# Optimization experiments

Hardware: AMD Instinct MI355X
Metric: run time of the kernel (lower is better)

The kernel has to match this reference:

```python
import jax, jax.numpy as jnp
import numpy as np

VOCAB = 32000
EMB = 10
HID = 256
CLS = 10
B = 1024
T = 256


def setup_inputs() -> dict:
    key = jax.random.key(0)
    ks = jax.random.split(key, 12)
    def w(k, shape):
        fan_in = shape[1]  # torch kaiming_normal_ (fan_in = size(1), gain=1 for 'linear')
        return jax.random.normal(k, shape, dtype=jnp.float32) / jnp.sqrt(jnp.float32(fan_in))
    inp = {
        "x": jax.random.randint(ks[0], (B, 1, T), 0, VOCAB, dtype=jnp.int32),
        "emb": jax.random.normal(ks[1], (VOCAB, EMB), dtype=jnp.float32),
        "Wgx": w(ks[2], (EMB, HID)), "Wgh": w(ks[3], (HID, HID)), "bg": jnp.zeros((HID,), jnp.float32),
        "Wix": w(ks[4], (EMB, HID)), "Wih": w(ks[5], (HID, HID)), "bi": jnp.zeros((HID,), jnp.float32),
        "Wfx": w(ks[6], (EMB, HID)), "Wfh": w(ks[7], (HID, HID)), "bf": jnp.zeros((HID,), jnp.float32),
        "Wox": w(ks[8], (EMB, HID)), "Woh": w(ks[9], (HID, HID)), "bo": jnp.zeros((HID,), jnp.float32),
        "Wph": w(ks[10], (HID, CLS)), "bp": jnp.zeros((CLS,), jnp.float32),
    }
    return inp


def reference(x, emb, Wgx, Wgh, bg, Wix, Wih, bi, Wfx, Wfh, bf, Wox, Woh, bo, Wph, bp):
    # Fuse the 4 gate projections into single matmuls (same math, concatenated).
    Wx = jnp.concatenate([Wgx, Wix, Wfx, Wox], axis=1)  # [EMB, 4H]
    Wh = jnp.concatenate([Wgh, Wih, Wfh, Woh], axis=1)  # [HID, 4H]
    b = jnp.concatenate([bg, bi, bf, bo], axis=0)       # [4H]
    H = Wgh.shape[0]
    tokens = x[:, 0, :].T  # [T, B] int

    def step(carry, tok_t):
        h, c = carry
        x_t = emb[tok_t]                       # [B, EMB]
        z = x_t @ Wx + h @ Wh + b              # [B, 4H]
        g = jnp.tanh(z[:, 0 * H:1 * H])
        i = jax.nn.sigmoid(z[:, 1 * H:2 * H])
        f = jax.nn.sigmoid(z[:, 2 * H:3 * H])
        o = jax.nn.sigmoid(z[:, 3 * H:4 * H])
        c = g * i + c * f
        h = jnp.tanh(c) * o
        return (h, c), None

    Bn = x.shape[0]
    h0 = jnp.zeros((Bn, H), dtype=emb.dtype)
    c0 = jnp.zeros((Bn, H), dtype=emb.dtype)
    (h, c), _ = jax.lax.scan(step, (h0, c0), tokens)
    return h @ Wph + bp  # [B, num_classes]
```

## Files before the change

### kernel.cpp

```cpp
#include <hip/hip_runtime.h>
#include <stdint.h>

#define T_STEPS 256
#define EMBD 10
#define NKIT 9
#define NBLK_K1 (64 * NKIT)
#define NBLK 256

typedef __attribute__((ext_vector_type(8))) short bf16x8;
typedef __attribute__((ext_vector_type(4))) float f32x4;
typedef __attribute__((ext_vector_type(4))) int   i32x4;

__device__ __forceinline__ unsigned short f2bf(float f) {
    union { float f; unsigned int u; } v; v.f = f;
    unsigned int u = v.u;
    unsigned int r = (u + 0x7FFFu + ((u >> 16) & 1u)) >> 16;
    return (unsigned short)r;
}
__device__ __forceinline__ float sig_fast(float x) {
    return __builtin_amdgcn_rcpf(1.0f + __builtin_amdgcn_exp2f(-1.4426950408889634f * x));
}
__device__ __forceinline__ float tanh_fast(float x) {
    return 1.0f - 2.0f * __builtin_amdgcn_rcpf(__builtin_amdgcn_exp2f(2.8853900817779268f * x) + 1.0f);
}
__device__ __forceinline__ f32x4 mfma_v(i32x4 a, i32x4 b, f32x4 c) {
    return __builtin_amdgcn_mfma_f32_16x16x32_bf16(
        __builtin_bit_cast(bf16x8, a), __builtin_bit_cast(bf16x8, b), c, 0, 0, 0);
}

__global__ __launch_bounds__(64) void build_wswz(
    const float* __restrict__ Wgx, const float* __restrict__ Wgh, const float* __restrict__ bg,
    const float* __restrict__ Wix, const float* __restrict__ Wih, const float* __restrict__ bi,
    const float* __restrict__ Wfx, const float* __restrict__ Wfh, const float* __restrict__ bf_,
    const float* __restrict__ Wox, const float* __restrict__ Woh, const float* __restrict__ bo,
    unsigned short* __restrict__ wswz, unsigned int* __restrict__ hxcz)
{
    {
        int4 z4 = {0, 0, 0, 0};
        size_t gid = (size_t)blockIdx.x * 64 + threadIdx.x;
        for (size_t i = gid; i < 131072; i += (size_t)NBLK_K1 * 64)
            ((int4*)hxcz)[i] = z4;
    }

    int g   = blockIdx.x / NKIT;
    int kit = blockIdx.x % NKIT;
    int lane = threadIdx.x;
    int n = g * 16 + (lane & 15);
    int q = n >> 8;
    int col = n & 255;
    const float* Wh = (q == 0) ? Wgh : (q == 1) ? Wih : (q == 2) ? Wfh : Woh;
    const float* Wx = (q == 0) ? Wgx : (q == 1) ? Wix : (q == 2) ? Wfx : Wox;
    const float* bb = (q == 0) ? bg  : (q == 1) ? bi  : (q == 2) ? bf_ : bo;
    int k0 = kit * 32 + (lane >> 4) * 8;

    int4 out;
    unsigned short* p = (unsigned short*)&out;
#pragma unroll
    for (int jx = 0; jx < 8; jx++) {
        int k = k0 + jx;
        float v = 0.0f;
        if (k < 256)             v = Wh[k * 256 + col];
        else if (k < 256 + EMBD) v = Wx[(k - 256) * 256 + col];
        else if (k == 266)       v = bb[col];
        p[jx] = f2bf(v);
    }
    ((int4*)wswz)[(kit * 64 + g) * 64 + lane] = out;
}

#define KIDX(s) ((s) == 7 ? 5 : (s))
#define BSRC(s, g) ((s) == 5 ? B_lds[(0 * 16 + (g) * 4 + j) * 64 + lane] \
                  : (s) == 6 ? B_lds[(1 * 16 + (g) * 4 + j) * 64 + lane] \
                  : breg[KIDX(s)][(g)])
#define DO_KIT(s) do { i32x4 a_ = ((const i32x4*)Ah_lds)[ah_rd + (s) * 4]; \
        acc0 = mfma_v(a_, BSRC(s, 0), acc0); \
        acc1 = mfma_v(a_, BSRC(s, 1), acc1); \
        acc2 = mfma_v(a_, BSRC(s, 2), acc2); \
        acc3 = mfma_v(a_, BSRC(s, 3), acc3); } while (0)

__global__ __launch_bounds__(256)
__attribute__((amdgpu_waves_per_eu(1)))
void lstm_main(
    const int*   __restrict__ xtok,
    const float* __restrict__ emb,
    const float* __restrict__ Wph,
    const float* __restrict__ bp,
    const unsigned short* __restrict__ wswz,
    unsigned long long* __restrict__ hxc,
    float* __restrict__ out)
{
    __shared__ __align__(16) unsigned short A8_lds[2][64 * 8];
    __shared__ __align__(16) i32x4 B_lds[2 * 16 * 64];
    __shared__ __align__(16) unsigned int Ah_lds[16 * 132];
    __shared__ float hbuf[16][68];
    __shared__ float outacc[160];

    const int tid  = threadIdx.x;
    const int j    = tid >> 6;
    const int lane = tid & 63;
    const int qq   = lane >> 4;
    const int col15 = lane & 15;
    const int blk  = blockIdx.x;
    const int gb   = blk & 63;
    const int hg   = blk >> 6;

    const int m_x = tid >> 4;
    const int e_x = tid & 15;

    const i32x4* Bg = (const i32x4*)wswz;

    i32x4 breg[7][4];
    {
        const int ks[7] = {0, 1, 2, 3, 4, 7, 8};
#pragma unroll
        for (int i = 0; i < 7; i++)
#pragma unroll
            for (int g = 0; g < 4; g++)
                breg[i][g] = Bg[(ks[i] * 64 + g * 16 + hg * 4 + j) * 64 + lane];
    }
    for (int i = tid; i < 2 * 16 * 64; i += 256) {
        int k   = i >> 10;
        int ntl = (i >> 6) & 15;
        int ln  = i & 63;
        int g_ = ntl >> 2, jj = ntl & 3;
        B_lds[i] = Bg[((5 + k) * 64 + g_ * 16 + hg * 4 + jj) * 64 + ln];
    }

    {
        int4 z4 = {0, 0, 0, 0};
        if (tid < 128) ((int4*)A8_lds)[tid] = z4;
    }
    __syncthreads();
    if (tid < 16) {
        A8_lds[0][(16 + tid) * 8 + 2] = 0x3F80;
        A8_lds[1][(16 + tid) * 8 + 2] = 0x3F80;
    }
    if (e_x < EMBD) {
        int tok = xtok[(gb * 16 + m_x) * T_STEPS + 0];
        float v = emb[tok * EMBD + e_x];
        A8_lds[0][(m_x + 16 * (e_x >> 3)) * 8 + (e_x & 7)] = f2bf(v);
    }
    __syncthreads();

    float c0 = 0.f, c1 = 0.f, c2 = 0.f, c3 = 0.f;

    const int ah_rd = (lane & 15) * 33 + (lane >> 4);
    const int c_loc = tid >> 2;
    const int rp0   = (tid & 3) * 2;
    const int rq0 = (hg + 1) & 3, rq1 = (hg + 2) & 3, rq2 = (hg + 3) & 3;
    const int c_own = hg * 64 + j * 16 + col15;
    unsigned short* AhS = (unsigned short*)Ah_lds;

    for (int t = 0; t < T_STEPS; t++) {
        const int p = t & 1, q = (t + 1) & 1;

        float xval = 0.0f;
        const bool do_x = (t < T_STEPS - 1) && (e_x < EMBD);
        if (t < T_STEPS - 1) {
            int tok = xtok[(gb * 16 + m_x) * T_STEPS + (t + 1)];
            if (e_x < EMBD) xval = emb[tok * EMBD + e_x];
        }

        const unsigned long long* hb = hxc + (size_t)(p * 64 + gb) * 2048;
        const unsigned long long* a0 = hb + (rq0 * 64 + c_loc) * 8 + rp0;
        const unsigned long long* a1 = hb + (rq1 * 64 + c_loc) * 8 + rp0;
        const unsigned long long* a2 = hb + (rq2 * 64 + c_loc) * 8 + rp0;
        i32x4 va, vb, vc;

        if (t > 0) {
            asm volatile("global_load_dwordx4 %0, %3, off sc1\n\t"
                         "global_load_dwordx4 %1, %4, off sc1\n\t"
                         "global_load_dwordx4 %2, %5, off sc1"
                         : "=&v"(va), "=&v"(vb), "=&v"(vc)
                         : "v"(a0), "v"(a1), "v"(a2) : "memory");
        }

        asm volatile("s_waitcnt lgkmcnt(0)" ::: "memory");
        __builtin_amdgcn_s_barrier();

        f32x4 acc0 = (f32x4){0.f, 0.f, 0.f, 0.f};
        f32x4 acc1 = (f32x4){0.f, 0.f, 0.f, 0.f};
        f32x4 acc2 = (f32x4){0.f, 0.f, 0.f, 0.f};
        f32x4 acc3 = (f32x4){0.f, 0.f, 0.f, 0.f};
        {
            i32x4 a8 = ((const i32x4*)A8_lds[p])[lane];
            acc0 = mfma_v(a8, breg[6][0], acc0);
            acc1 = mfma_v(a8, breg[6][1], acc1);
            acc2 = mfma_v(a8, breg[6][2], acc2);
            acc3 = mfma_v(a8, breg[6][3], acc3);
        }

        if (t > 0) {
            if      (hg == 0) { DO_KIT(0); DO_KIT(1); }
            else if (hg == 1) { DO_KIT(2); DO_KIT(3); }
            else if (hg == 2) { DO_KIT(4); DO_KIT(5); }
            else              { DO_KIT(6); DO_KIT(7); }

            asm volatile("s_waitcnt vmcnt(0)"
                         : "+v"(va), "+v"(vb), "+v"(vc) :: "memory");
            int spins = 0;
            while ((va.y != t || va.w != t || vb.y != t || vb.w != t ||
                    vc.y != t || vc.w != t) && spins < 20000) {
                ++spins;
                __builtin_amdgcn_s_sleep(1);
                asm volatile("global_load_dwordx4 %0, %3, off sc1\n\t"
                             "global_load_dwordx4 %1, %4, off sc1\n\t"
                             "global_load_dwordx4 %2, %5, off sc1\n\t"
                             "s_waitcnt vmcnt(0)"
                             : "=&v"(va), "=&v"(vb), "=&v"(vc)
                             : "v"(a0), "v"(a1), "v"(a2) : "memory");
            }
            {
                const int r0 = 2 * rp0;
                int cg0 = rq0 * 64 + c_loc;
                AhS[(r0 + 0) * 264 + cg0] = (unsigned short)(va.x & 0xffff);
                AhS[(r0 + 1) * 264 + cg0] = (unsigned short)((unsigned)va.x >> 16);
                AhS[(r0 + 2) * 264 + cg0] = (unsigned short)(va.z & 0xffff);
                AhS[(r0 + 3) * 264 + cg0] = (unsigned short)((unsigned)va.z >> 16);
                int cg1 = rq1 * 64 + c_loc;
                AhS[(r0 + 0) * 264 + cg1] = (unsigned short)(vb.x & 0xffff);
                AhS[(r0 + 1) * 264 + cg1] = (unsigned short)((unsigned)vb.x >> 16);
                AhS[(r0 + 2) * 264 + cg1] = (unsigned short)(vb.z & 0xffff);
                AhS[(r0 + 3) * 264 + cg1] = (unsigned short)((unsigned)vb.z >> 16);
                int cg2 = rq2 * 64 + c_loc;
                AhS[(r0 + 0) * 264 + cg2] = (unsigned short)(vc.x & 0xffff);
                AhS[(r0 + 1) * 264 + cg2] = (unsigned short)((unsigned)vc.x >> 16);
                AhS[(r0 + 2) * 264 + cg2] = (unsigned short)(vc.z & 0xffff);
                AhS[(r0 + 3) * 264 + cg2] = (unsigned short)((unsigned)vc.z >> 16);
            }
            asm volatile("s_waitcnt lgkmcnt(0)" ::: "memory");
            __builtin_amdgcn_s_barrier();

            if (hg != 0) { DO_KIT(0); DO_KIT(1); }
            if (hg != 1) { DO_KIT(2); DO_KIT(3); }
            if (hg != 2) { DO_KIT(4); DO_KIT(5); }
            if (hg != 3) { DO_KIT(6); DO_KIT(7); }
        }

        float h0, h1, h2, h3;
        {
            float gg, ii, ff, oo, cn;
            gg = tanh_fast(acc0[0]); ii = sig_fast(acc1[0]);
            ff = sig_fast(acc2[0]);  oo = sig_fast(acc3[0]);
            cn = gg * ii + c0 * ff; c0 = cn; h0 = tanh_fast(cn) * oo;
            gg = tanh_fast(acc0[1]); ii = sig_fast(acc1[1]);
            ff = sig_fast(acc2[1]);  oo = sig_fast(acc3[1]);
            cn = gg * ii + c1 * ff; c1 = cn; h1 = tanh_fast(cn) * oo;
            gg = tanh_fast(acc0[2]); ii = sig_fast(acc1[2]);
            ff = sig_fast(acc2[2]);  oo = sig_fast(acc3[2]);
            cn = gg * ii + c2 * ff; c2 = cn; h2 = tanh_fast(cn) * oo;
            gg = tanh_fast(acc0[3]); ii = sig_fast(acc1[3]);
            ff = sig_fast(acc2[3]);  oo = sig_fast(acc3[3]);
            cn = gg * ii + c3 * ff; c3 = cn; h3 = tanh_fast(cn) * oo;
        }

        if (t < T_STEPS - 1) {
            unsigned int p01, p23;
            asm("v_cvt_pk_bf16_f32 %0, %1, %2" : "=v"(p01) : "v"(h0), "v"(h1));
            asm("v_cvt_pk_bf16_f32 %0, %1, %2" : "=v"(p23) : "v"(h2), "v"(h3));
            AhS[(4 * qq + 0) * 264 + c_own] = (unsigned short)(p01 & 0xffff);
            AhS[(4 * qq + 1) * 264 + c_own] = (unsigned short)(p01 >> 16);
            AhS[(4 * qq + 2) * 264 + c_own] = (unsigned short)(p23 & 0xffff);
            AhS[(4 * qq + 3) * 264 + c_own] = (unsigned short)(p23 >> 16);
            if (do_x)
                A8_lds[q][(m_x + 16 * (e_x >> 3)) * 8 + (e_x & 7)] = f2bf(xval);
            i32x4 pv;
            pv.x = (int)p01; pv.y = t + 1; pv.z = (int)p23; pv.w = t + 1;
            unsigned long long* dst =
                hxc + (size_t)(q * 64 + gb) * 2048 + (size_t)c_own * 8 + 2 * qq;
            asm volatile("global_store_dwordx4 %0, %1, off sc1"
                         :: "v"(dst), "v"(pv) : "memory");
        } else {
            hbuf[4 * qq + 0][j * 16 + col15] = h0;
            hbuf[4 * qq + 1][j * 16 + col15] = h1;
            hbuf[4 * qq + 2][j * 16 + col15] = h2;
            hbuf[4 * qq + 3][j * 16 + col15] = h3;
            if (tid < 160) outacc[tid] = 0.0f;
            __syncthreads();
            if (tid < 160) {
                int m = tid / 10, cl = tid - m * 10;
                float s = 0.0f;
#pragma unroll 8
                for (int c = 0; c < 64; c++)
                    s += hbuf[m][c] * Wph[(hg * 64 + c) * 10 + cl];
                if (hg == 0) s += bp[cl];
                atomicAdd(&out[(gb * 16 + m) * 10 + cl], s);
            }
        }
    }
}

extern "C" void kernel_launch(void* const* d_in, const int* in_sizes, int n_in,
                              void* d_out, int out_size, void* d_ws, size_t ws_size,
                              hipStream_t stream) {
    const int*   x    = (const int*)  d_in[0];
    const float* emb  = (const float*)d_in[1];
    const float* Wgx  = (const float*)d_in[2];
    const float* Wgh  = (const float*)d_in[3];
    const float* bg   = (const float*)d_in[4];
    const float* Wix  = (const float*)d_in[5];
    const float* Wih  = (const float*)d_in[6];
    const float* bi   = (const float*)d_in[7];
    const float* Wfx  = (const float*)d_in[8];
    const float* Wfh  = (const float*)d_in[9];
    const float* bf_  = (const float*)d_in[10];
    const float* Wox  = (const float*)d_in[11];
    const float* Woh  = (const float*)d_in[12];
    const float* bo   = (const float*)d_in[13];
    const float* Wph  = (const float*)d_in[14];
    const float* bp   = (const float*)d_in[15];

    char* ws = (char*)d_ws;
    unsigned short*     wswz = (unsigned short*)ws;
    unsigned long long* hxc  = (unsigned long long*)(ws + 589824 + 4096);

    build_wswz<<<NBLK_K1, 64, 0, stream>>>(Wgx, Wgh, bg, Wix, Wih, bi,
                                           Wfx, Wfh, bf_, Wox, Woh, bo,
                                           wswz, (unsigned int*)hxc);
    lstm_main<<<NBLK, 256, 0, stream>>>(x, emb, Wph, bp, wswz, hxc,
                                        (float*)d_out);
}
```

Before: 555.2 us.

## Add dedicated poller wave to prefetch next-step hidden state into double-buffered LDS

Adds a fifth wave per block (320 threads) that spins on the global exchange buffer for the next step's hidden-state slices from the other three blocks and writes them into a double-buffered LDS tile. The four compute waves then run all eight MFMA k-iterations from LDS, with a single barrier per step. The aim is to take global polling and LDS scatter off the compute waves' critical path and drop the intra-step split and second barrier. In exchange there is an extra wave per block, doubled Ah LDS, and the waves_per_eu(1) attribute is removed, which may change register allocation for the 28 preloaded B fragments.

```diff
diff --git a/kernel.cpp b/kernel.cpp
--- a/kernel.cpp
+++ b/kernel.cpp
@@ -71,14 +71,13 @@
 #define BSRC(s, g) ((s) == 5 ? B_lds[(0 * 16 + (g) * 4 + j) * 64 + lane] \
                   : (s) == 6 ? B_lds[(1 * 16 + (g) * 4 + j) * 64 + lane] \
                   : breg[KIDX(s)][(g)])
-#define DO_KIT(s) do { i32x4 a_ = ((const i32x4*)Ah_lds)[ah_rd + (s) * 4]; \
+#define DO_KIT(s) do { i32x4 a_ = Ahp[ah_rd + (s) * 4]; \
         acc0 = mfma_v(a_, BSRC(s, 0), acc0); \
         acc1 = mfma_v(a_, BSRC(s, 1), acc1); \
         acc2 = mfma_v(a_, BSRC(s, 2), acc2); \
         acc3 = mfma_v(a_, BSRC(s, 3), acc3); } while (0)
 
-__global__ __launch_bounds__(256)
-__attribute__((amdgpu_waves_per_eu(1)))
+__global__ __launch_bounds__(320)
 void lstm_main(
     const int*   __restrict__ xtok,
     const float* __restrict__ emb,
@@ -90,9 +89,8 @@
 {
     __shared__ __align__(16) unsigned short A8_lds[2][64 * 8];
     __shared__ __align__(16) i32x4 B_lds[2 * 16 * 64];
-    __shared__ __align__(16) unsigned int Ah_lds[16 * 132];
+    __shared__ __align__(16) unsigned int Ah_lds[2][16 * 132];
     __shared__ float hbuf[16][68];
-    __shared__ float outacc[160];
 
     const int tid  = threadIdx.x;
     const int j    = tid >> 6;
@@ -102,6 +100,7 @@
     const int blk  = blockIdx.x;
     const int gb   = blk & 63;
     const int hg   = blk >> 6;
+    const bool is_comp = (tid < 256);
 
     const int m_x = tid >> 4;
     const int e_x = tid & 15;
@@ -109,7 +108,7 @@
     const i32x4* Bg = (const i32x4*)wswz;
 
     i32x4 breg[7][4];
-    {
+    if (is_comp) {
         const int ks[7] = {0, 1, 2, 3, 4, 7, 8};
 #pragma unroll
         for (int i = 0; i < 7; i++)
@@ -117,7 +116,7 @@
             for (int g = 0; g < 4; g++)
                 breg[i][g] = Bg[(ks[i] * 64 + g * 16 + hg * 4 + j) * 64 + lane];
     }
-    for (int i = tid; i < 2 * 16 * 64; i += 256) {
+    for (int i = tid; i < 2 * 16 * 64; i += 320) {
         int k   = i >> 10;
         int ntl = (i >> 6) & 15;
         int ln  = i & 63;
@@ -134,7 +133,7 @@
         A8_lds[0][(16 + tid) * 8 + 2] = 0x3F80;
         A8_lds[1][(16 + tid) * 8 + 2] = 0x3F80;
     }
-    if (e_x < EMBD) {
+    if (is_comp && e_x < EMBD) {
         int tok = xtok[(gb * 16 + m_x) * T_STEPS + 0];
         float v = emb[tok * EMBD + e_x];
         A8_lds[0][(m_x + 16 * (e_x >> 3)) * 8 + (e_x & 7)] = f2bf(v);
@@ -144,148 +143,138 @@
     float c0 = 0.f, c1 = 0.f, c2 = 0.f, c3 = 0.f;
 
     const int ah_rd = (lane & 15) * 33 + (lane >> 4);
-    const int c_loc = tid >> 2;
-    const int rp0   = (tid & 3) * 2;
-    const int rq0 = (hg + 1) & 3, rq1 = (hg + 2) & 3, rq2 = (hg + 3) & 3;
     const int c_own = hg * 64 + j * 16 + col15;
-    unsigned short* AhS = (unsigned short*)Ah_lds;
+
+    const int ptid = tid - 256;
+    int offv[12];
+#pragma unroll
+    for (int i = 0; i < 12; i++) {
+        int e   = ptid * 24 + 2 * i;
+        int rqi = e >> 9;
+        offv[i] = (rqi + (rqi >= hg ? 1 : 0)) * 512 + (e & 511);
+    }
 
     for (int t = 0; t < T_STEPS; t++) {
         const int p = t & 1, q = (t + 1) & 1;
 
-        float xval = 0.0f;
-        const bool do_x = (t < T_STEPS - 1) && (e_x < EMBD);
+        if (is_comp) {
+            float xval = 0.0f;
+            const bool do_x = (t < T_STEPS - 1) && (e_x < EMBD);
+            if (t < T_STEPS - 1) {
+                int tok = xtok[(gb * 16 + m_x) * T_STEPS + (t + 1)];
+                if (e_x < EMBD) xval = emb[tok * EMBD + e_x];
+            }
+
+            f32x4 acc0 = (f32x4){0.f, 0.f, 0.f, 0.f};
+            f32x4 acc1 = (f32x4){0.f, 0.f, 0.f, 0.f};
+            f32x4 acc2 = (f32x4){0.f, 0.f, 0.f, 0.f};
+            f32x4 acc3 = (f32x4){0.f, 0.f, 0.f, 0.f};
+            {
+                i32x4 a8 = ((const i32x4*)A8_lds[p])[lane];
+                acc0 = mfma_v(a8, breg[6][0], acc0);
+                acc1 = mfma_v(a8, breg[6][1], acc1);
+                acc2 = mfma_v(a8, breg[6][2], acc2);
+                acc3 = mfma_v(a8, breg[6][3], acc3);
+            }
+            if (t > 0) {
+                const i32x4* Ahp = (const i32x4*)Ah_lds[p];
+                DO_KIT(0); DO_KIT(1); DO_KIT(2); DO_KIT(3);
+                DO_KIT(4); DO_KIT(5); DO_KIT(6); DO_KIT(7);
+            }
+
+            float h0, h1, h2, h3;
+            {
+                float gg, ii, ff, oo, cn;
+                gg = tanh_fast(acc0[0]); ii = sig_fast(acc1[0]);
+                ff = sig_fast(acc2[0]);  oo = sig_fast(acc3[0]);
+                cn = gg * ii + c0 * ff; c0 = cn; h0 = tanh_fast(cn) * oo;
+                gg = tanh_fast(acc0[1]); ii = sig_fast(acc1[1]);
+                ff = sig_fast(acc2[1]);  oo = sig_fast(acc3[1]);
+                cn = gg * ii + c1 * ff; c1 = cn; h1 = tanh_fast(cn) * oo;
+                gg = tanh_fast(acc0[2]); ii = sig_fast(acc1[2]);
+                ff = sig_fast(acc2[2]);  oo = sig_fast(acc3[2]);
+                cn = gg * ii + c2 * ff; c2 = cn; h2 = tanh_fast(cn) * oo;
+                gg = tanh_fast(acc0[3]); ii = sig_fast(acc1[3]);
+                ff = sig_fast(acc2[3]);  oo = sig_fast(acc3[3]);
+                cn = gg * ii + c3 * ff; c3 = cn; h3 = tanh_fast(cn) * oo;
+            }
+
+            if (t < T_STEPS - 1) {
+                unsigned int p01, p23;
+                asm("v_cvt_pk_bf16_f32 %0, %1, %2" : "=v"(p01) : "v"(h0), "v"(h1));
+                asm("v_cvt_pk_bf16_f32 %0, %1, %2" : "=v"(p23) : "v"(h2), "v"(h3));
+                unsigned short* AqS = (unsigned short*)Ah_lds[q];
+                AqS[(4 * qq + 0) * 264 + c_own] = (unsigned short)(p01 & 0xffff);
+                AqS[(4 * qq + 1) * 264 + c_own] = (unsigned short)(p01 >> 16);
+                AqS[(4 * qq + 2) * 264 + c_own] = (unsigned short)(p23 & 0xffff);
+                AqS[(4 * qq + 3) * 264 + c_own] = (unsigned short)(p23 >> 16);
+                if (do_x)
+                    A8_lds[q][(m_x + 16 * (e_x >> 3)) * 8 + (e_x & 7)] = f2bf(xval);
+                i32x4 pv;
+                pv.x = (int)p01; pv.y = t + 1; pv.z = (int)p23; pv.w = t + 1;
+                unsigned long long* dst =
+                    hxc + (size_t)(q * 64 + gb) * 2048 + (size_t)c_own * 8 + 2 * qq;
+                asm volatile("global_store_dwordx4 %0, %1, off sc1"
+                             :: "v"(dst), "v"(pv) : "memory");
+            } else {
+                hbuf[4 * qq + 0][j * 16 + col15] = h0;
+                hbuf[4 * qq + 1][j * 16 + col15] = h1;
+                hbuf[4 * qq + 2][j * 16 + col15] = h2;
+                hbuf[4 * qq + 3][j * 16 + col15] = h3;
+            }
+        } else {
+            if (t < T_STEPS - 1) {
+                const unsigned long long* hbq =
+                    hxc + (size_t)(q * 64 + gb) * 2048;
+                const unsigned s_exp = (unsigned)(t + 1);
+                i32x4 pv[12];
+                int spins = 0;
+                for (;;) {
+#pragma unroll
+                    for (int i = 0; i < 12; i++)
+                        asm volatile("global_load_dwordx4 %0, %1, off sc1"
+                                     : "=&v"(pv[i]) : "v"(hbq + offv[i]) : "memory");
+                    asm volatile("s_waitcnt vmcnt(0)"
+                                 : "+v"(pv[0]), "+v"(pv[1]), "+v"(pv[2]), "+v"(pv[3]),
+                                   "+v"(pv[4]), "+v"(pv[5]), "+v"(pv[6]), "+v"(pv[7]),
+                                   "+v"(pv[8]), "+v"(pv[9]), "+v"(pv[10]), "+v"(pv[11])
+                                 :: "memory");
+                    unsigned bad = 0;
+#pragma unroll
+                    for (int i = 0; i < 12; i++)
+                        bad |= ((unsigned)pv[i].y ^ s_exp) | ((unsigned)pv[i].w ^ s_exp);
+                    if (!bad || spins >= 20000) break;
+                    ++spins;
+                    __builtin_amdgcn_s_sleep(1);
+                }
+                unsigned short* AqS = (unsigned short*)Ah_lds[q];
+#pragma unroll
+                for (int i = 0; i < 12; i++) {
+                    const int cg = offv[i] >> 3;
+                    const int r0 = (offv[i] & 7) * 2;
+                    AqS[(r0 + 0) * 264 + cg] = (unsigned short)(pv[i].x & 0xffff);
+                    AqS[(r0 + 1) * 264 + cg] = (unsigned short)((unsigned)pv[i].x >> 16);
+                    AqS[(r0 + 2) * 264 + cg] = (unsigned short)(pv[i].z & 0xffff);
+                    AqS[(r0 + 3) * 264 + cg] = (unsigned short)((unsigned)pv[i].z >> 16);
+                }
+            }
+        }
+
         if (t < T_STEPS - 1) {
-            int tok = xtok[(gb * 16 + m_x) * T_STEPS + (t + 1)];
-            if (e_x < EMBD) xval = emb[tok * EMBD + e_x];
-        }
-
-        const unsigned long long* hb = hxc + (size_t)(p * 64 + gb) * 2048;
-        const unsigned long long* a0 = hb + (rq0 * 64 + c_loc) * 8 + rp0;
-        const unsigned long long* a1 = hb + (rq1 * 64 + c_loc) * 8 + rp0;
-        const unsigned long long* a2 = hb + (rq2 * 64 + c_loc) * 8 + rp0;
-        i32x4 va, vb, vc;
-
-        if (t > 0) {
-            asm volatile("global_load_dwordx4 %0, %3, off sc1\n\t"
-                         "global_load_dwordx4 %1, %4, off sc1\n\t"
-                         "global_load_dwordx4 %2, %5, off sc1"
-                         : "=&v"(va), "=&v"(vb), "=&v"(vc)
-                         : "v"(a0), "v"(a1), "v"(a2) : "memory");
-        }
-
-        asm volatile("s_waitcnt lgkmcnt(0)" ::: "memory");
-        __builtin_amdgcn_s_barrier();
-
-        f32x4 acc0 = (f32x4){0.f, 0.f, 0.f, 0.f};
-        f32x4 acc1 = (f32x4){0.f, 0.f, 0.f, 0.f};
-        f32x4 acc2 = (f32x4){0.f, 0.f, 0.f, 0.f};
-        f32x4 acc3 = (f32x4){0.f, 0.f, 0.f, 0.f};
-        {
-            i32x4 a8 = ((const i32x4*)A8_lds[p])[lane];
-            acc0 = mfma_v(a8, breg[6][0], acc0);
-            acc1 = mfma_v(a8, breg[6][1], acc1);
-            acc2 = mfma_v(a8, breg[6][2], acc2);
-            acc3 = mfma_v(a8, breg[6][3], acc3);
-        }
-
-        if (t > 0) {
-            if      (hg == 0) { DO_KIT(0); DO_KIT(1); }
-            else if (hg == 1) { DO_KIT(2); DO_KIT(3); }
-            else if (hg == 2) { DO_KIT(4); DO_KIT(5); }
-            else              { DO_KIT(6); DO_KIT(7); }
-
-            asm volatile("s_waitcnt vmcnt(0)"
-                         : "+v"(va), "+v"(vb), "+v"(vc) :: "memory");
-            int spins = 0;
-            while ((va.y != t || va.w != t || vb.y != t || vb.w != t ||
-                    vc.y != t || vc.w != t) && spins < 20000) {
-                ++spins;
-                __builtin_amdgcn_s_sleep(1);
-                asm volatile("global_load_dwordx4 %0, %3, off sc1\n\t"
-                             "global_load_dwordx4 %1, %4, off sc1\n\t"
-                             "global_load_dwordx4 %2, %5, off sc1\n\t"
-                             "s_waitcnt vmcnt(0)"
-                             : "=&v"(va), "=&v"(vb), "=&v"(vc)
-                             : "v"(a0), "v"(a1), "v"(a2) : "memory");
-            }
-            {
-                const int r0 = 2 * rp0;
-                int cg0 = rq0 * 64 + c_loc;
-                AhS[(r0 + 0) * 264 + cg0] = (unsigned short)(va.x & 0xffff);
-                AhS[(r0 + 1) * 264 + cg0] = (unsigned short)((unsigned)va.x >> 16);
-                AhS[(r0 + 2) * 264 + cg0] = (unsigned short)(va.z & 0xffff);
-                AhS[(r0 + 3) * 264 + cg0] = (unsigned short)((unsigned)va.z >> 16);
-                int cg1 = rq1 * 64 + c_loc;
-                AhS[(r0 + 0) * 264 + cg1] = (unsigned short)(vb.x & 0xffff);
-                AhS[(r0 + 1) * 264 + cg1] = (unsigned short)((unsigned)vb.x >> 16);
-                AhS[(r0 + 2) * 264 + cg1] = (unsigned short)(vb.z & 0xffff);
-                AhS[(r0 + 3) * 264 + cg1] = (unsigned short)((unsigned)vb.z >> 16);
-                int cg2 = rq2 * 64 + c_loc;
-                AhS[(r0 + 0) * 264 + cg2] = (unsigned short)(vc.x & 0xffff);
-                AhS[(r0 + 1) * 264 + cg2] = (unsigned short)((unsigned)vc.x >> 16);
-                AhS[(r0 + 2) * 264 + cg2] = (unsigned short)(vc.z & 0xffff);
-                AhS[(r0 + 3) * 264 + cg2] = (unsigned short)((unsigned)vc.z >> 16);
-            }
             asm volatile("s_waitcnt lgkmcnt(0)" ::: "memory");
             __builtin_amdgcn_s_barrier();
-
-            if (hg != 0) { DO_KIT(0); DO_KIT(1); }
-            if (hg != 1) { DO_KIT(2); DO_KIT(3); }
-            if (hg != 2) { DO_KIT(4); DO_KIT(5); }
-            if (hg != 3) { DO_KIT(6); DO_KIT(7); }
         }
-
-        float h0, h1, h2, h3;
-        {
-            float gg, ii, ff, oo, cn;
-            gg = tanh_fast(acc0[0]); ii = sig_fast(acc1[0]);
-            ff = sig_fast(acc2[0]);  oo = sig_fast(acc3[0]);
-            cn = gg * ii + c0 * ff; c0 = cn; h0 = tanh_fast(cn) * oo;
-            gg = tanh_fast(acc0[1]); ii = sig_fast(acc1[1]);
-            ff = sig_fast(acc2[1]);  oo = sig_fast(acc3[1]);
-            cn = gg * ii + c1 * ff; c1 = cn; h1 = tanh_fast(cn) * oo;
-            gg = tanh_fast(acc0[2]); ii = sig_fast(acc1[2]);
-            ff = sig_fast(acc2[2]);  oo = sig_fast(acc3[2]);
-            cn = gg * ii + c2 * ff; c2 = cn; h2 = tanh_fast(cn) * oo;
-            gg = tanh_fast(acc0[3]); ii = sig_fast(acc1[3]);
-            ff = sig_fast(acc2[3]);  oo = sig_fast(acc3[3]);
-            cn = gg * ii + c3 * ff; c3 = cn; h3 = tanh_fast(cn) * oo;
-        }
-
-        if (t < T_STEPS - 1) {
-            unsigned int p01, p23;
-            asm("v_cvt_pk_bf16_f32 %0, %1, %2" : "=v"(p01) : "v"(h0), "v"(h1));
-            asm("v_cvt_pk_bf16_f32 %0, %1, %2" : "=v"(p23) : "v"(h2), "v"(h3));
-            AhS[(4 * qq + 0) * 264 + c_own] = (unsigned short)(p01 & 0xffff);
-            AhS[(4 * qq + 1) * 264 + c_own] = (unsigned short)(p01 >> 16);
-            AhS[(4 * qq + 2) * 264 + c_own] = (unsigned short)(p23 & 0xffff);
-            AhS[(4 * qq + 3) * 264 + c_own] = (unsigned short)(p23 >> 16);
-            if (do_x)
-                A8_lds[q][(m_x + 16 * (e_x >> 3)) * 8 + (e_x & 7)] = f2bf(xval);
-            i32x4 pv;
-            pv.x = (int)p01; pv.y = t + 1; pv.z = (int)p23; pv.w = t + 1;
-            unsigned long long* dst =
-                hxc + (size_t)(q * 64 + gb) * 2048 + (size_t)c_own * 8 + 2 * qq;
-            asm volatile("global_store_dwordx4 %0, %1, off sc1"
-                         :: "v"(dst), "v"(pv) : "memory");
-        } else {
-            hbuf[4 * qq + 0][j * 16 + col15] = h0;
-            hbuf[4 * qq + 1][j * 16 + col15] = h1;
-            hbuf[4 * qq + 2][j * 16 + col15] = h2;
-            hbuf[4 * qq + 3][j * 16 + col15] = h3;
-            if (tid < 160) outacc[tid] = 0.0f;
-            __syncthreads();
-            if (tid < 160) {
-                int m = tid / 10, cl = tid - m * 10;
-                float s = 0.0f;
+    }
+
+    __syncthreads();
+    if (tid < 160) {
+        int m = tid / 10, cl = tid - m * 10;
+        float s = 0.0f;
 #pragma unroll 8
-                for (int c = 0; c < 64; c++)
-                    s += hbuf[m][c] * Wph[(hg * 64 + c) * 10 + cl];
-                if (hg == 0) s += bp[cl];
-                atomicAdd(&out[(gb * 16 + m) * 10 + cl], s);
-            }
-        }
+        for (int c = 0; c < 64; c++)
+            s += hbuf[m][c] * Wph[(hg * 64 + c) * 10 + cl];
+        if (hg == 0) s += bp[cl];
+        atomicAdd(&out[(gb * 16 + m) * 10 + cl], s);
     }
 }
 
@@ -316,6 +305,6 @@
     build_wswz<<<NBLK_K1, 64, 0, stream>>>(Wgx, Wgh, bg, Wix, Wih, bi,
                                            Wfx, Wfh, bf_, Wox, Woh, bo,
                                            wswz, (unsigned int*)hxc);
-    lstm_main<<<NBLK, 256, 0, stream>>>(x, emb, Wph, bp, wswz, hxc,
+    lstm_main<<<NBLK, 320, 0, stream>>>(x, emb, Wph, bp, wswz, hxc,
                                         (float*)d_out);
 }
```

Result: slower. 1.348 ms (+142.7%).
